# Kernel tuning notes

Hardware: AMD Instinct MI355X
Metric: run time of the kernel (lower is better)

Reference implementation:

```python
import jax, jax.numpy as jnp
import numpy as np

N_NODES = 50000
N_EDGES = 800000
D_IN = 128
D_OUT = 128


def setup_inputs() -> dict:
    key = jax.random.key(0)
    k_feat, k_src, k_dst, k_ws, k_bs, k_wn = jax.random.split(key, 6)
    feat = jax.random.normal(k_feat, (N_NODES, D_IN), dtype=jnp.float32)
    src = jax.random.randint(k_src, (N_EDGES,), 0, N_NODES, dtype=jnp.int64)
    dst = jax.random.randint(k_dst, (N_EDGES,), 0, N_NODES, dtype=jnp.int64)
    # fc_self: Linear(D_IN, D_OUT, bias=True); fc_neigh: Linear(D_IN, D_OUT, bias=False)
    W_self = jax.random.normal(k_ws, (D_OUT, D_IN), dtype=jnp.float32) * (1.0 / np.sqrt(D_IN))
    b_self = jax.random.normal(k_bs, (D_OUT,), dtype=jnp.float32) * 0.01
    # xavier_uniform with relu gain
    gain = float(np.sqrt(2.0))
    bound = gain * float(np.sqrt(6.0 / (D_IN + D_OUT)))
    W_neigh = jax.random.uniform(k_wn, (D_OUT, D_IN), dtype=jnp.float32, minval=-bound, maxval=bound)
    bias = jnp.zeros((D_OUT,), dtype=jnp.float32)
    return {"feat": feat, "src": src, "dst": dst, "W_self": W_self,
            "b_self": b_self, "W_neigh": W_neigh, "bias": bias}


def reference(feat, src, dst, W_self, b_self, W_neigh, bias):
    # copy_u('h','m') + fn.mean('m','neigh'): gather src feats, mean-reduce by dst.
    # lin_before_mp is False (in_feats == out_feats), so aggregate raw feats first.
    n = feat.shape[0]
    msgs = feat[src]                                             # [E, D_IN]
    neigh_sum = jax.ops.segment_sum(msgs, dst, num_segments=n)   # [N, D_IN]
    deg = jax.ops.segment_sum(jnp.ones(src.shape, feat.dtype), dst, num_segments=n)
    # DGL mean yields 0 for zero-in-degree nodes
    h_neigh = jnp.where(deg[:, None] > 0, neigh_sum / jnp.maximum(deg, 1.0)[:, None], 0.0)
    h_neigh = h_neigh @ W_neigh.T                                # fc_neigh (no bias)
    h_self = feat @ W_self.T + b_self                            # fc_self
    return h_self + h_neigh + bias
```

## Files before the change

kernel.cpp:

```cpp
#include <hip/hip_runtime.h>
#include <hip/hip_fp8.h>

#define N_NODES 50000
#define N_EDGES 800000
#define D 128
#define NBUK 196
#define CAPR 4591
#define CAPP 6400
#define PCHUNK 2048
#define PBLOCKS 392

typedef __bf16 bf16x8 __attribute__((ext_vector_type(8)));
typedef __bf16 bf16x4 __attribute__((ext_vector_type(4)));
typedef float  f32x4  __attribute__((ext_vector_type(4)));
typedef float  f32x2  __attribute__((ext_vector_type(2)));

#if defined(__has_builtin)
#if __has_builtin(__builtin_amdgcn_cvt_pk_f32_fp8) && __has_builtin(__builtin_amdgcn_cvt_pk_fp8_f32)
#define HW_FP8 1
#endif
#endif

#define OFF_GCURSOR   0ull
#define OFF_OFFS      1024ull
#define OFF_PACKED    201216ull
#define OFF_FEAT8     5218816ull
#define OFF_WC16      11618944ull
#define OFF_BIASC     11684480ull
#define OFF_FEAT16    11684992ull

__global__ __launch_bounds__(256)
void partition_kernel(const int* __restrict__ src, const int* __restrict__ dst,
                      int* __restrict__ gcursor, int* __restrict__ packed, int n) {
    __shared__ int lh[NBUK];
    __shared__ int lbase[NBUK];
    const int tid = threadIdx.x;
    const int e0 = blockIdx.x * PCHUNK;
    int d[8], s[8];
    for (int i = tid; i < NBUK; i += 256) lh[i] = 0;
    __syncthreads();
    #pragma unroll
    for (int j = 0; j < 8; ++j) {
        int e = e0 + j * 256 + tid;
        bool ok = e < n;
        d[j] = ok ? dst[e] : -1;
        s[j] = ok ? src[e] : 0;
        if (ok) atomicAdd(&lh[d[j] >> 8], 1);
    }
    __syncthreads();
    for (int i = tid; i < NBUK; i += 256) {
        int c = lh[i];
        lbase[i] = c ? atomicAdd(&gcursor[i], c) : 0;
    }
    __syncthreads();
    for (int i = tid; i < NBUK; i += 256) lh[i] = 0;
    __syncthreads();
    #pragma unroll
    for (int j = 0; j < 8; ++j) {
        if (d[j] >= 0) {
            int b = d[j] >> 8;
            int r = atomicAdd(&lh[b], 1);
            int pos = lbase[b] + r;
            if (pos < CAPR)
                packed[b * CAPP + pos] = ((d[j] & 255) << 16) | s[j];
        }
    }
}

__global__ __launch_bounds__(256)
void mix_kernel(int* __restrict__ packed, const int* __restrict__ gcursor,
                int* __restrict__ offs,
                const float* __restrict__ feat, unsigned char* __restrict__ feat8,
                __bf16* __restrict__ feat16,
                const float* __restrict__ Ws, const float* __restrict__ Wn,
                const float* __restrict__ b_self, const float* __restrict__ bias,
                __bf16* __restrict__ Wc16, float* __restrict__ biasc) {
    __shared__ int pk[CAPR];
    __shared__ int srt[CAPP];
    __shared__ int lh[256];
    __shared__ int loff[256];
    __shared__ int ws5[5];
    const int tid = threadIdx.x;
    if (blockIdx.x < NBUK) {
        const int lane = tid & 63;
        const int wv = tid >> 6;
        const int b = blockIdx.x;
        const int node0 = b * 256;
        const int ncnt = min(256, N_NODES - node0);
        const int base = b * CAPP;
        const int cnt = min(gcursor[b], CAPR);

        for (int i = tid; i < cnt; i += 256) pk[i] = packed[base + i];
        lh[tid] = 0;
        __syncthreads();
        for (int i = tid; i < cnt; i += 256)
            atomicAdd(&lh[pk[i] >> 16], 1);
        __syncthreads();
        int c  = lh[tid];
        int cp = (c + 7) & ~7;
        int v = cp;
        #pragma unroll
        for (int o = 1; o < 64; o <<= 1) {
            int u = __shfl_up(v, o);
            if (lane >= o) v += u;
        }
        if (lane == 63) ws5[wv] = v;
        __syncthreads();
        if (tid == 0) {
            int r = 0;
            #pragma unroll
            for (int j = 0; j < 4; ++j) { int t = ws5[j]; ws5[j] = r; r += t; }
            ws5[4] = r;
        }
        __syncthreads();
        int ex = ws5[wv] + (v - cp);
        loff[tid] = ex;
        lh[tid] = 0;
        __syncthreads();
        for (int i = tid; i < cnt; i += 256) {
            int p = pk[i];
            int l = p >> 16;
            int r = atomicAdd(&lh[l], 1);
            srt[loff[l] + r] = p & 0xFFFF;
        }
        for (int j = c; j < cp; ++j) srt[ex + j] = N_NODES;
        __syncthreads();
        const int ptot = ws5[4];
        for (int i = tid; i < ptot; i += 256) packed[base + i] = srt[i];
        if (tid < ncnt) offs[node0 + tid] = (ex << 16) | c;
    } else if (blockIdx.x < NBUK + 3125) {
        size_t i = ((size_t)(blockIdx.x - NBUK) * 256 + tid) * 8;
        float4 f0 = *(const float4*)(feat + i);
        float4 f1 = *(const float4*)(feat + i + 4);
        bf16x8 t16;
        t16[0]=(__bf16)f0.x; t16[1]=(__bf16)f0.y; t16[2]=(__bf16)f0.z; t16[3]=(__bf16)f0.w;
        t16[4]=(__bf16)f1.x; t16[5]=(__bf16)f1.y; t16[6]=(__bf16)f1.z; t16[7]=(__bf16)f1.w;
        *(bf16x8*)(feat16 + i) = t16;
#ifdef HW_FP8
        int q0 = __builtin_amdgcn_cvt_pk_fp8_f32(f0.x, f0.y, 0, false);
        q0     = __builtin_amdgcn_cvt_pk_fp8_f32(f0.z, f0.w, q0, true);
        int q1 = __builtin_amdgcn_cvt_pk_fp8_f32(f1.x, f1.y, 0, false);
        q1     = __builtin_amdgcn_cvt_pk_fp8_f32(f1.z, f1.w, q1, true);
        uint2 qq; qq.x = (unsigned)q0; qq.y = (unsigned)q1;
        *(uint2*)(feat8 + i) = qq;
#else
        float fv[8] = {f0.x, f0.y, f0.z, f0.w, f1.x, f1.y, f1.z, f1.w};
        union { unsigned char b[8]; unsigned long long u; } q;
        #pragma unroll
        for (int j = 0; j < 8; ++j) { __hip_fp8_e4m3 e(fv[j]); q.b[j] = e.__x; }
        *(unsigned long long*)(feat8 + i) = q.u;
#endif
    } else if (blockIdx.x < NBUK + 3157) {
        int idx = (blockIdx.x - NBUK - 3125) * 256 + tid;
        int col = idx >> 6;
        int kq  = (idx & 63) * 4;
        const float* srcp = (kq < D) ? (Ws + (size_t)col * D + kq)
                                     : (Wn + (size_t)col * D + (kq - D));
        float4 f = *(const float4*)srcp;
        bf16x4 t;
        t[0]=(__bf16)f.x; t[1]=(__bf16)f.y; t[2]=(__bf16)f.z; t[3]=(__bf16)f.w;
        *(bf16x4*)(Wc16 + (size_t)col * 256 + kq) = t;
    } else {
        if (tid < D) biasc[tid] = b_self[tid] + bias[tid];
        else if (tid < D + 32)
            ((unsigned*)(feat8 + (size_t)N_NODES * D))[tid - 128] = 0u;
    }
}

__device__ __forceinline__ float fp8tof_sw(unsigned char b) {
    __hip_fp8_e4m3 t; t.__x = b;
    return (float)t;
}

__global__ __launch_bounds__(512)
void fused_kernel(const __bf16* __restrict__ feat16,
                  const unsigned char* __restrict__ feat8,
                  const int* __restrict__ offs,
                  const int* __restrict__ csr,
                  const __bf16* __restrict__ Wc16,
                  const float* __restrict__ biasc,
                  float* __restrict__ out) {
    __shared__ __bf16 At[64][264];
    const int tid = threadIdx.x;
    const int node0 = blockIdx.x * 64;

    for (int idx = tid; idx < 1024; idx += 512) {
        int row = idx >> 4;
        int seg = (idx & 15) * 8;
        int n = node0 + row;
        bf16x8 t = {};
        if (n < N_NODES) t = *(const bf16x8*)(feat16 + (size_t)n * D + seg);
        *(bf16x8*)&At[row][seg] = t;
    }

    {
        const int hw = tid >> 5;
        const int lane = tid & 31;
        const unsigned int* g8 = (const unsigned int*)feat8;
        int ovs[4];
        #pragma unroll
        for (int t = 0; t < 4; ++t) {
            int n = node0 + hw + t * 16;
            ovs[t] = (n < N_NODES) ? offs[n] : 0;
        }
        #pragma unroll
        for (int t = 0; t < 4; ++t) {
            int i = hw + t * 16;
            int n = node0 + i;
            int dg = ovs[t] & 0xFFFF;
            int dgp = (dg + 7) & ~7;
            float a0 = 0.f, a1 = 0.f, a2 = 0.f, a3 = 0.f;
            if (n < N_NODES && dg > 0) {
                const int* lst = csr + (n >> 8) * CAPP + (ovs[t] >> 16);
                for (int j = 0; j < dgp; j += 8) {
                    int s[8]; unsigned int w[8];
                    #pragma unroll
                    for (int q = 0; q < 8; ++q) s[q] = lst[j + q];
                    #pragma unroll
                    for (int q = 0; q < 8; ++q)
                        w[q] = g8[(size_t)s[q] * 32 + lane];
                    #pragma unroll
                    for (int q = 0; q < 8; ++q) {
#ifdef HW_FP8
                        f32x2 lo = __builtin_amdgcn_cvt_pk_f32_fp8((int)w[q], false);
                        f32x2 hi = __builtin_amdgcn_cvt_pk_f32_fp8((int)w[q], true);
                        a0 += lo[0]; a1 += lo[1]; a2 += hi[0]; a3 += hi[1];
#else
                        a0 += fp8tof_sw(w[q] & 0xFF);
                        a1 += fp8tof_sw((w[q] >> 8) & 0xFF);
                        a2 += fp8tof_sw((w[q] >> 16) & 0xFF);
                        a3 += fp8tof_sw(w[q] >> 24);
#endif
                    }
                }
            }
            float sc = dg > 0 ? 1.0f / (float)dg : 0.f;
            bf16x4 hv;
            hv[0] = (__bf16)(a0 * sc); hv[1] = (__bf16)(a1 * sc);
            hv[2] = (__bf16)(a2 * sc); hv[3] = (__bf16)(a3 * sc);
            *(bf16x4*)&At[i][128 + lane * 4] = hv;
        }
    }
    __syncthreads();

    const int wv = tid >> 6;
    const int lane = tid & 63;
    const int m = lane & 15;
    const int quad = lane >> 4;
    const int r0 = (wv & 1) * 32;
    const int c0 = (wv >> 1) * 32;

    f32x4 acc[2][2] = {};
    #pragma unroll
    for (int k0 = 0; k0 < 256; k0 += 32) {
        const int kk = k0 + quad * 8;
        bf16x8 a0 = *(const bf16x8*)&At[r0 + m][kk];
        bf16x8 a1 = *(const bf16x8*)&At[r0 + 16 + m][kk];
        #pragma unroll
        for (int ct = 0; ct < 2; ++ct) {
            int col = c0 + ct * 16 + m;
            bf16x8 b = *(const bf16x8*)(Wc16 + (size_t)col * 256 + kk);
            acc[0][ct] = __builtin_amdgcn_mfma_f32_16x16x32_bf16(a0, b, acc[0][ct], 0, 0, 0);
            acc[1][ct] = __builtin_amdgcn_mfma_f32_16x16x32_bf16(a1, b, acc[1][ct], 0, 0, 0);
        }
    }
    __syncthreads();

    float* Ct = (float*)&At[0][0];
    #pragma unroll
    for (int rt = 0; rt < 2; ++rt) {
        #pragma unroll
        for (int ct = 0; ct < 2; ++ct) {
            int ccol = c0 + ct * 16 + m;
            int crow = r0 + rt * 16 + quad * 4;
            #pragma unroll
            for (int r = 0; r < 4; ++r)
                Ct[(crow + r) * 132 + ccol] = acc[rt][ct][r];
        }
    }
    __syncthreads();
    for (int idx = tid; idx < 64 * 32; idx += 512) {
        int row = idx >> 5;
        int c4 = (idx & 31) * 4;
        int n = node0 + row;
        if (n < N_NODES) {
            float4 v = *(float4*)&Ct[row * 132 + c4];
            float4 bb = *(const float4*)(biasc + c4);
            v.x += bb.x; v.y += bb.y; v.z += bb.z; v.w += bb.w;
            *(float4*)&out[(size_t)n * D + c4] = v;
        }
    }
}

extern "C" void kernel_launch(void* const* d_in, const int* in_sizes, int n_in,
                              void* d_out, int out_size, void* d_ws, size_t ws_size,
                              hipStream_t stream) {
    const float* feat    = (const float*)d_in[0];
    const int*   src     = (const int*)d_in[1];
    const int*   dst     = (const int*)d_in[2];
    const float* W_self  = (const float*)d_in[3];
    const float* b_self  = (const float*)d_in[4];
    const float* W_neigh = (const float*)d_in[5];
    const float* bias    = (const float*)d_in[6];
    float* out = (float*)d_out;
    char*  ws  = (char*)d_ws;

    int* gcursor = (int*)(ws + OFF_GCURSOR);
    int* offs    = (int*)(ws + OFF_OFFS);
    int* packed  = (int*)(ws + OFF_PACKED);
    unsigned char* feat8 = (unsigned char*)(ws + OFF_FEAT8);
    __bf16* Wc16   = (__bf16*)(ws + OFF_WC16);
    float*  biasc  = (float*)(ws + OFF_BIASC);
    __bf16* feat16 = (__bf16*)(ws + OFF_FEAT16);
    const int n_edges = in_sizes[1];

    hipMemsetAsync(gcursor, 0, 1024, stream);
    partition_kernel<<<dim3(PBLOCKS), 256, 0, stream>>>(src, dst, gcursor, packed, n_edges);
    mix_kernel<<<dim3(NBUK + 3158), 256, 0, stream>>>(packed, gcursor, offs,
                                                      feat, feat8, feat16,
                                                      W_self, W_neigh,
                                                      b_self, bias, Wc16, biasc);
    fused_kernel<<<dim3((N_NODES + 63) / 64), 512, 0, stream>>>(
        feat16, feat8, offs, packed, Wc16, biasc, out);
}
```

Baseline: 143.9 us.

## Replace two-pass bucket partition with per-node atomic fixed-capacity adjacency lists

Drops the bucketed partition kernel and the shared-memory sort pass in favour of a single scatter that does a global atomicAdd on each destination's degree counter and writes the source into a fixed 64-slot row per node. The bf16 copy of feat is no longer produced; the fused kernel converts fp32 feat to bf16 itself while loading its self tile. The change removes one kernel launch and the bf16 feature write and read. In exchange it adds 800k contended global atomics, scattered 4-byte writes, and a 12.8MB CSR array, and it silently truncates any node whose in-degree exceeds 64.

```diff
diff --git a/kernel.cpp b/kernel.cpp
--- a/kernel.cpp
+++ b/kernel.cpp
@@ -4,11 +4,11 @@
 #define N_NODES 50000
 #define N_EDGES 800000
 #define D 128
-#define NBUK 196
-#define CAPR 4591
-#define CAPP 6400
+#define CAPN 64
 #define PCHUNK 2048
-#define PBLOCKS 392
+#define SCAT_BLOCKS 391
+#define FEAT_BLOCKS 3125
+#define W_BLOCKS 32
 
 typedef __bf16 bf16x8 __attribute__((ext_vector_type(8)));
 typedef __bf16 bf16x4 __attribute__((ext_vector_type(4)));
@@ -21,121 +21,43 @@
 #endif
 #endif
 
-#define OFF_GCURSOR   0ull
-#define OFF_OFFS      1024ull
-#define OFF_PACKED    201216ull
-#define OFF_FEAT8     5218816ull
-#define OFF_WC16      11618944ull
-#define OFF_BIASC     11684480ull
-#define OFF_FEAT16    11684992ull
+#define OFF_DEGC   0ull
+#define OFF_CSR    200704ull
+#define OFF_FEAT8  13000704ull
+#define OFF_WC16   19400960ull
+#define OFF_BIASC  19466496ull
+
+__device__ __forceinline__ float fp8tof_sw(unsigned char b) {
+    __hip_fp8_e4m3 t; t.__x = b;
+    return (float)t;
+}
 
 __global__ __launch_bounds__(256)
-void partition_kernel(const int* __restrict__ src, const int* __restrict__ dst,
-                      int* __restrict__ gcursor, int* __restrict__ packed, int n) {
-    __shared__ int lh[NBUK];
-    __shared__ int lbase[NBUK];
+void prep_kernel(const int* __restrict__ src, const int* __restrict__ dst,
+                 int* __restrict__ degc, int* __restrict__ csr,
+                 const float* __restrict__ feat, unsigned char* __restrict__ feat8,
+                 const float* __restrict__ Ws, const float* __restrict__ Wn,
+                 const float* __restrict__ b_self, const float* __restrict__ bias,
+                 __bf16* __restrict__ Wc16, float* __restrict__ biasc, int n) {
     const int tid = threadIdx.x;
-    const int e0 = blockIdx.x * PCHUNK;
-    int d[8], s[8];
-    for (int i = tid; i < NBUK; i += 256) lh[i] = 0;
-    __syncthreads();
-    #pragma unroll
-    for (int j = 0; j < 8; ++j) {
-        int e = e0 + j * 256 + tid;
-        bool ok = e < n;
-        d[j] = ok ? dst[e] : -1;
-        s[j] = ok ? src[e] : 0;
-        if (ok) atomicAdd(&lh[d[j] >> 8], 1);
-    }
-    __syncthreads();
-    for (int i = tid; i < NBUK; i += 256) {
-        int c = lh[i];
-        lbase[i] = c ? atomicAdd(&gcursor[i], c) : 0;
-    }
-    __syncthreads();
-    for (int i = tid; i < NBUK; i += 256) lh[i] = 0;
-    __syncthreads();
-    #pragma unroll
-    for (int j = 0; j < 8; ++j) {
-        if (d[j] >= 0) {
-            int b = d[j] >> 8;
-            int r = atomicAdd(&lh[b], 1);
-            int pos = lbase[b] + r;
-            if (pos < CAPR)
-                packed[b * CAPP + pos] = ((d[j] & 255) << 16) | s[j];
-        }
-    }
-}
-
-__global__ __launch_bounds__(256)
-void mix_kernel(int* __restrict__ packed, const int* __restrict__ gcursor,
-                int* __restrict__ offs,
-                const float* __restrict__ feat, unsigned char* __restrict__ feat8,
-                __bf16* __restrict__ feat16,
-                const float* __restrict__ Ws, const float* __restrict__ Wn,
-                const float* __restrict__ b_self, const float* __restrict__ bias,
-                __bf16* __restrict__ Wc16, float* __restrict__ biasc) {
-    __shared__ int pk[CAPR];
-    __shared__ int srt[CAPP];
-    __shared__ int lh[256];
-    __shared__ int loff[256];
-    __shared__ int ws5[5];
-    const int tid = threadIdx.x;
-    if (blockIdx.x < NBUK) {
-        const int lane = tid & 63;
-        const int wv = tid >> 6;
-        const int b = blockIdx.x;
-        const int node0 = b * 256;
-        const int ncnt = min(256, N_NODES - node0);
-        const int base = b * CAPP;
-        const int cnt = min(gcursor[b], CAPR);
-
-        for (int i = tid; i < cnt; i += 256) pk[i] = packed[base + i];
-        lh[tid] = 0;
-        __syncthreads();
-        for (int i = tid; i < cnt; i += 256)
-            atomicAdd(&lh[pk[i] >> 16], 1);
-        __syncthreads();
-        int c  = lh[tid];
-        int cp = (c + 7) & ~7;
-        int v = cp;
-        #pragma unroll
-        for (int o = 1; o < 64; o <<= 1) {
-            int u = __shfl_up(v, o);
-            if (lane >= o) v += u;
-        }
-        if (lane == 63) ws5[wv] = v;
-        __syncthreads();
-        if (tid == 0) {
-            int r = 0;
-            #pragma unroll
-            for (int j = 0; j < 4; ++j) { int t = ws5[j]; ws5[j] = r; r += t; }
-            ws5[4] = r;
-        }
-        __syncthreads();
-        int ex = ws5[wv] + (v - cp);
-        loff[tid] = ex;
-        lh[tid] = 0;
-        __syncthreads();
-        for (int i = tid; i < cnt; i += 256) {
-            int p = pk[i];
-            int l = p >> 16;
-            int r = atomicAdd(&lh[l], 1);
-            srt[loff[l] + r] = p & 0xFFFF;
-        }
-        for (int j = c; j < cp; ++j) srt[ex + j] = N_NODES;
-        __syncthreads();
-        const int ptot = ws5[4];
-        for (int i = tid; i < ptot; i += 256) packed[base + i] = srt[i];
-        if (tid < ncnt) offs[node0 + tid] = (ex << 16) | c;
-    } else if (blockIdx.x < NBUK + 3125) {
-        size_t i = ((size_t)(blockIdx.x - NBUK) * 256 + tid) * 8;
+    const int bid = blockIdx.x;
+    if (bid < SCAT_BLOCKS) {
+        const int e0 = bid * PCHUNK + tid;
+        #pragma unroll
+        for (int j = 0; j < 8; ++j) {
+            int e = e0 + j * 256;
+            if (e < n) {
+                int d = dst[e];
+                int s = src[e];
+                int pos = atomicAdd(&degc[d], 1);
+                if (pos < CAPN)
+                    csr[(size_t)d * CAPN + pos] = s;
+            }
+        }
+    } else if (bid < SCAT_BLOCKS + FEAT_BLOCKS) {
+        size_t i = ((size_t)(bid - SCAT_BLOCKS) * 256 + tid) * 8;
         float4 f0 = *(const float4*)(feat + i);
         float4 f1 = *(const float4*)(feat + i + 4);
-        bf16x8 t16;
-        t16[0]=(__bf16)f0.x; t16[1]=(__bf16)f0.y; t16[2]=(__bf16)f0.z; t16[3]=(__bf16)f0.w;
-        t16[4]=(__bf16)f1.x; t16[5]=(__bf16)f1.y; t16[6]=(__bf16)f1.z; t16[7]=(__bf16)f1.w;
-        *(bf16x8*)(feat16 + i) = t16;
 #ifdef HW_FP8
         int q0 = __builtin_amdgcn_cvt_pk_fp8_f32(f0.x, f0.y, 0, false);
         q0     = __builtin_amdgcn_cvt_pk_fp8_f32(f0.z, f0.w, q0, true);
@@ -150,8 +72,8 @@
         for (int j = 0; j < 8; ++j) { __hip_fp8_e4m3 e(fv[j]); q.b[j] = e.__x; }
         *(unsigned long long*)(feat8 + i) = q.u;
 #endif
-    } else if (blockIdx.x < NBUK + 3157) {
-        int idx = (blockIdx.x - NBUK - 3125) * 256 + tid;
+    } else if (bid < SCAT_BLOCKS + FEAT_BLOCKS + W_BLOCKS) {
+        int idx = (bid - SCAT_BLOCKS - FEAT_BLOCKS) * 256 + tid;
         int col = idx >> 6;
         int kq  = (idx & 63) * 4;
         const float* srcp = (kq < D) ? (Ws + (size_t)col * D + kq)
@@ -167,15 +89,10 @@
     }
 }
 
-__device__ __forceinline__ float fp8tof_sw(unsigned char b) {
-    __hip_fp8_e4m3 t; t.__x = b;
-    return (float)t;
-}
-
 __global__ __launch_bounds__(512)
-void fused_kernel(const __bf16* __restrict__ feat16,
+void fused_kernel(const float* __restrict__ feat,
                   const unsigned char* __restrict__ feat8,
-                  const int* __restrict__ offs,
+                  const int* __restrict__ degc,
                   const int* __restrict__ csr,
                   const __bf16* __restrict__ Wc16,
                   const float* __restrict__ biasc,
@@ -187,9 +104,15 @@
     for (int idx = tid; idx < 1024; idx += 512) {
         int row = idx >> 4;
         int seg = (idx & 15) * 8;
-        int n = node0 + row;
+        int nn = node0 + row;
         bf16x8 t = {};
-        if (n < N_NODES) t = *(const bf16x8*)(feat16 + (size_t)n * D + seg);
+        if (nn < N_NODES) {
+            const float* fp = feat + (size_t)nn * D + seg;
+            float4 f0 = *(const float4*)fp;
+            float4 f1 = *(const float4*)(fp + 4);
+            t[0]=(__bf16)f0.x; t[1]=(__bf16)f0.y; t[2]=(__bf16)f0.z; t[3]=(__bf16)f0.w;
+            t[4]=(__bf16)f1.x; t[5]=(__bf16)f1.y; t[6]=(__bf16)f1.z; t[7]=(__bf16)f1.w;
+        }
         *(bf16x8*)&At[row][seg] = t;
     }
 
@@ -197,25 +120,25 @@
         const int hw = tid >> 5;
         const int lane = tid & 31;
         const unsigned int* g8 = (const unsigned int*)feat8;
-        int ovs[4];
+        int dgs[4];
         #pragma unroll
         for (int t = 0; t < 4; ++t) {
-            int n = node0 + hw + t * 16;
-            ovs[t] = (n < N_NODES) ? offs[n] : 0;
+            int nn = node0 + hw + t * 16;
+            dgs[t] = (nn < N_NODES) ? min(degc[nn], CAPN) : 0;
         }
         #pragma unroll
         for (int t = 0; t < 4; ++t) {
             int i = hw + t * 16;
-            int n = node0 + i;
-            int dg = ovs[t] & 0xFFFF;
-            int dgp = (dg + 7) & ~7;
+            int nn = node0 + i;
+            int dg = dgs[t];
             float a0 = 0.f, a1 = 0.f, a2 = 0.f, a3 = 0.f;
-            if (n < N_NODES && dg > 0) {
-                const int* lst = csr + (n >> 8) * CAPP + (ovs[t] >> 16);
-                for (int j = 0; j < dgp; j += 8) {
+            if (dg > 0) {
+                const int* lst = csr + (size_t)nn * CAPN;
+                for (int j = 0; j < dg; j += 8) {
                     int s[8]; unsigned int w[8];
                     #pragma unroll
-                    for (int q = 0; q < 8; ++q) s[q] = lst[j + q];
+                    for (int q = 0; q < 8; ++q)
+                        s[q] = (j + q < dg) ? lst[j + q] : N_NODES;
                     #pragma unroll
                     for (int q = 0; q < 8; ++q)
                         w[q] = g8[(size_t)s[q] * 32 + lane];
@@ -282,12 +205,12 @@
     for (int idx = tid; idx < 64 * 32; idx += 512) {
         int row = idx >> 5;
         int c4 = (idx & 31) * 4;
-        int n = node0 + row;
-        if (n < N_NODES) {
+        int nn = node0 + row;
+        if (nn < N_NODES) {
             float4 v = *(float4*)&Ct[row * 132 + c4];
             float4 bb = *(const float4*)(biasc + c4);
             v.x += bb.x; v.y += bb.y; v.z += bb.z; v.w += bb.w;
-            *(float4*)&out[(size_t)n * D + c4] = v;
+            *(float4*)&out[(size_t)nn * D + c4] = v;
         }
     }
 }
@@ -305,21 +228,16 @@
     float* out = (float*)d_out;
     char*  ws  = (char*)d_ws;
 
-    int* gcursor = (int*)(ws + OFF_GCURSOR);
-    int* offs    = (int*)(ws + OFF_OFFS);
-    int* packed  = (int*)(ws + OFF_PACKED);
+    int* degc = (int*)(ws + OFF_DEGC);
+    int* csr  = (int*)(ws + OFF_CSR);
     unsigned char* feat8 = (unsigned char*)(ws + OFF_FEAT8);
-    __bf16* Wc16   = (__bf16*)(ws + OFF_WC16);
-    float*  biasc  = (float*)(ws + OFF_BIASC);
-    __bf16* feat16 = (__bf16*)(ws + OFF_FEAT16);
+    __bf16* Wc16  = (__bf16*)(ws + OFF_WC16);
+    float*  biasc = (float*)(ws + OFF_BIASC);
     const int n_edges = in_sizes[1];
 
-    hipMemsetAsync(gcursor, 0, 1024, stream);
-    partition_kernel<<<dim3(PBLOCKS), 256, 0, stream>>>(src, dst, gcursor, packed, n_edges);
-    mix_kernel<<<dim3(NBUK + 3158), 256, 0, stream>>>(packed, gcursor, offs,
-                                                      feat, feat8, feat16,
-                                                      W_self, W_neigh,
-                                                      b_self, bias, Wc16, biasc);
+    hipMemsetAsync(degc, 0, 200704, stream);
+    prep_kernel<<<dim3(SCAT_BLOCKS + FEAT_BLOCKS + W_BLOCKS + 1), 256, 0, stream>>>(
+        src, dst, degc, csr, feat, feat8, W_self, W_neigh, b_self, bias, Wc16, biasc, n_edges);
     fused_kernel<<<dim3((N_NODES + 63) / 64), 512, 0, stream>>>(
-        feat16, feat8, offs, packed, Wc16, biasc, out);
-}
+        feat, feat8, degc, csr, Wc16, biasc, out);
+}
```

Result: slower. 181.0 us (+25.8%).
